# Optimization experiments

Hardware: AMD Instinct MI355X
Metric: run time of the kernel (lower is better)

## Reference

```python
import jax, jax.numpy as jnp
import numpy as np

E, H, F = 8, 1024, 4096  # experts, hidden_size, ffn_hidden_size
INIT_STD = 0.02


def setup_inputs() -> dict:
    key = jax.random.key(0)
    kx, k1, k2 = jax.random.split(key, 3)
    total_tokens = 16384
    x = jax.random.normal(kx, (total_tokens, H), dtype=jnp.float32)
    w1 = jax.random.normal(k1, (E, H, F), dtype=jnp.float32) * INIT_STD
    w2 = jax.random.normal(k2, (E, F, H), dtype=jnp.float32) * INIT_STD
    return {"x": x, "w1": w1, "w2": w2, "rows_per_expert": total_tokens // E}


def reference(x, w1, w2, rows_per_expert):
    # Grouped GEMM 1: per-expert x_e @ w1[e]  -> [E, T, F]
    e, h = w1.shape[0], w1.shape[1]
    xg = x.reshape(e, rows_per_expert, h)          # tokens grouped by expert
    inter = jnp.einsum('eth,ehf->etf', xg, w1)     # grouped GEMM 1
    inter = jax.nn.gelu(inter)                     # activation_fn
    out = jnp.einsum('etf,efh->eth', inter, w2)    # grouped GEMM 2
    return out.reshape(-1, h)
```

## Files before the change

### kernel.cpp

```cpp
#include <hip/hip_runtime.h>
#include <hip/hip_bf16.h>


typedef __attribute__((ext_vector_type(8))) short short8;
typedef __attribute__((ext_vector_type(4))) float floatx4;

static __device__ __forceinline__ ushort f2bf(float f) {
  __hip_bfloat16 h = __float2bfloat16(f);
  return *(ushort*)&h;
}

__global__ __launch_bounds__(256) void cvt_bf16(const float* __restrict__ in,
                                                __hip_bfloat16* __restrict__ out,
                                                int n4) {
  int i = blockIdx.x * 256 + threadIdx.x;
  if (i >= n4) return;
  float4 v = ((const float4*)in)[i];
  ushort4 u;
  u.x = f2bf(v.x); u.y = f2bf(v.y); u.z = f2bf(v.z); u.w = f2bf(v.w);
  ((ushort4*)out)[i] = u;
}

template<int K, int N>
__global__ __launch_bounds__(256) void tpose_bf16(const float* __restrict__ in,
                                                  __hip_bfloat16* __restrict__ out) {
  __shared__ __align__(16) ushort tile[64][66];
  const size_t eoff = (size_t)blockIdx.z * (size_t)K * N;
  const int n0 = blockIdx.x * 64;
  const int k0 = blockIdx.y * 64;
  const int t = threadIdx.x;
  const int g = t >> 4;
  const int j = t & 15;
#pragma unroll
  for (int p = 0; p < 2; ++p) {
    const int k = p * 32 + g * 2;
    const float4 a = *(const float4*)(in + eoff + (size_t)(k0 + k) * N + n0 + 4 * j);
    const float4 b = *(const float4*)(in + eoff + (size_t)(k0 + k + 1) * N + n0 + 4 * j);
#pragma unroll
    for (int i = 0; i < 4; ++i) {
      ushort2 u;
      u.x = f2bf(((const float*)&a)[i]);
      u.y = f2bf(((const float*)&b)[i]);
      *(ushort2*)&tile[4 * j + i][k] = u;
    }
  }
  __syncthreads();
#pragma unroll
  for (int p = 0; p < 4; ++p) {
    const int n = p * 16 + g;
    const ushort4 u = *(const ushort4*)&tile[n][4 * j];
    *(ushort4*)(out + eoff + (size_t)(n0 + n) * K + k0 + 4 * j) = u;
  }
}

template<bool GELU, typename OutT>
__global__ __launch_bounds__(256) void gemm_bt(const __hip_bfloat16* __restrict__ A,
                                               const __hip_bfloat16* __restrict__ Bt,
                                               OutT* __restrict__ C,
                                               int M, int N, int K) {
  __shared__ __align__(16) __hip_bfloat16 As[128 * 32];
  __shared__ __align__(16) __hip_bfloat16 Bs[128 * 32];

  const int e = blockIdx.z;
  A  += (size_t)e * M * K;
  Bt += (size_t)e * N * K;
  C  += (size_t)e * M * N;

  const int m0 = blockIdx.y * 128;
  const int n0 = blockIdx.x * 128;
  const int t = threadIdx.x;
  const int lane = t & 63;
  const int l16 = lane & 15;
  const int quad = lane >> 4;
  const int w = t >> 6;
  const int wr = (w >> 1) * 64;
  const int wc = (w & 1) * 64;

  floatx4 acc[4][4] = {};

  for (int k0 = 0; k0 < K; k0 += 32) {
    __syncthreads();
#pragma unroll
    for (int i = 0; i < 2; ++i) {
      const int id = t + i * 256;
      const int row = id >> 2;
      const int cc = (id & 3) * 8;
      __builtin_amdgcn_global_load_lds(
          (const __attribute__((address_space(1))) void*)(A + (size_t)(m0 + row) * K + k0 + cc),
          (__attribute__((address_space(3))) void*)(As + id * 8), 16, 0, 0);
    }
#pragma unroll
    for (int i = 0; i < 2; ++i) {
      const int id = t + i * 256;
      const int row = id >> 2;
      const int cc = (id & 3) * 8;
      __builtin_amdgcn_global_load_lds(
          (const __attribute__((address_space(1))) void*)(Bt + (size_t)(n0 + row) * K + k0 + cc),
          (__attribute__((address_space(3))) void*)(Bs + id * 8), 16, 0, 0);
    }
    __syncthreads();

    short8 af[4], bf[4];
#pragma unroll
    for (int i = 0; i < 4; ++i)
      af[i] = *(const short8*)(As + (wr + i * 16 + l16) * 32 + quad * 8);
#pragma unroll
    for (int j = 0; j < 4; ++j)
      bf[j] = *(const short8*)(Bs + (wc + j * 16 + l16) * 32 + quad * 8);
#pragma unroll
    for (int i = 0; i < 4; ++i)
#pragma unroll
      for (int j = 0; j < 4; ++j)
        acc[i][j] = __builtin_amdgcn_mfma_f32_16x16x32_bf16(af[i], bf[j], acc[i][j], 0, 0, 0);
  }

#pragma unroll
  for (int i = 0; i < 4; ++i) {
#pragma unroll
    for (int r = 0; r < 4; ++r) {
      const int row = m0 + wr + i * 16 + quad * 4 + r;
      OutT* crow = C + (size_t)row * N + n0 + wc + l16;
#pragma unroll
      for (int j = 0; j < 4; ++j) {
        float v = acc[i][j][r];
        if constexpr (GELU) {
          const float u2 = 1.5957691216057308f * (v + 0.044715f * v * v * v);
          const float ex = __expf(u2);
          v = v - v * __builtin_amdgcn_rcpf(ex + 1.0f);
        }
        if constexpr (sizeof(OutT) == 2)
          crow[j * 16] = __float2bfloat16(v);
        else
          crow[j * 16] = v;
      }
    }
  }
}

extern "C" void kernel_launch(void* const* d_in, const int* in_sizes, int n_in,
                              void* d_out, int out_size, void* d_ws, size_t ws_size,
                              hipStream_t stream) {
  const float* x  = (const float*)d_in[0];
  const float* w1 = (const float*)d_in[1];
  const float* w2 = (const float*)d_in[2];
  float* out = (float*)d_out;

  char* ws = (char*)d_ws;
  __hip_bfloat16* xb    = (__hip_bfloat16*)(ws);
  __hip_bfloat16* w1t   = (__hip_bfloat16*)(ws + (size_t)32 * 1024 * 1024);
  __hip_bfloat16* w2t   = (__hip_bfloat16*)(ws + (size_t)96 * 1024 * 1024);
  __hip_bfloat16* inter = (__hip_bfloat16*)(ws + (size_t)160 * 1024 * 1024);

  cvt_bf16<<<16384, 256, 0, stream>>>(x, xb, 16384 * 1024 / 4);
  tpose_bf16<1024, 4096><<<dim3(64, 16, 8), 256, 0, stream>>>(w1, w1t);
  tpose_bf16<4096, 1024><<<dim3(16, 64, 8), 256, 0, stream>>>(w2, w2t);
  gemm_bt<true, __hip_bfloat16>
      <<<dim3(32, 16, 8), 256, 0, stream>>>(xb, w1t, inter, 2048, 4096, 1024);
  gemm_bt<false, float>
      <<<dim3(8, 16, 8), 256, 0, stream>>>(inter, w2t, out, 2048, 1024, 4096);
}
```

Before: 760.8 us.

## Fuse input conversion and weight transposes into one prep kernel with swizzled LDS

Replaces the three separate preprocessing launches (x conversion, w1 transpose, w2 transpose) with one prep kernel that dispatches on block index. The transpose tiles grow to 128x64, each thread packs 8 bf16 values along K into a 16-byte store, and an XOR swizzle on the LDS layout replaces padding to avoid bank conflicts. This is meant to cut launch overhead and tail effects and to widen global stores, at the cost of more registers per thread and a larger shared-memory footprint per block.

```diff
diff --git a/kernel.cpp b/kernel.cpp
--- a/kernel.cpp
+++ b/kernel.cpp
@@ -10,46 +10,76 @@
   return *(ushort*)&h;
 }
 
-__global__ __launch_bounds__(256) void cvt_bf16(const float* __restrict__ in,
-                                                __hip_bfloat16* __restrict__ out,
-                                                int n4) {
-  int i = blockIdx.x * 256 + threadIdx.x;
-  if (i >= n4) return;
-  float4 v = ((const float4*)in)[i];
-  ushort4 u;
-  u.x = f2bf(v.x); u.y = f2bf(v.y); u.z = f2bf(v.z); u.w = f2bf(v.w);
-  ((ushort4*)out)[i] = u;
+static __device__ __forceinline__ int swz(int n, int o) {
+  return o ^ (n & 7) ^ ((n >> 3) & 7);
 }
 
 template<int K, int N>
-__global__ __launch_bounds__(256) void tpose_bf16(const float* __restrict__ in,
-                                                  __hip_bfloat16* __restrict__ out) {
-  __shared__ __align__(16) ushort tile[64][66];
-  const size_t eoff = (size_t)blockIdx.z * (size_t)K * N;
-  const int n0 = blockIdx.x * 64;
-  const int k0 = blockIdx.y * 64;
+static __device__ __forceinline__ void tpose_tile(const float* __restrict__ in,
+                                                  __hip_bfloat16* __restrict__ out,
+                                                  ushort* lds, int e, int nt, int kt) {
+  const size_t eoff = (size_t)e * K * N;
+  const int n0 = nt * 128, k0 = kt * 64;
   const int t = threadIdx.x;
+  const int j = t & 15;
   const int g = t >> 4;
-  const int j = t & 15;
+  const int o = g >> 1;
+  const int h = g & 1;
+  const float* src = in + eoff + (size_t)(k0 + 8 * o) * N + n0 + h * 64 + 4 * j;
+  float4 v[8];
 #pragma unroll
-  for (int p = 0; p < 2; ++p) {
-    const int k = p * 32 + g * 2;
-    const float4 a = *(const float4*)(in + eoff + (size_t)(k0 + k) * N + n0 + 4 * j);
-    const float4 b = *(const float4*)(in + eoff + (size_t)(k0 + k + 1) * N + n0 + 4 * j);
+  for (int r = 0; r < 8; ++r)
+    v[r] = *(const float4*)(src + (size_t)r * N);
 #pragma unroll
-    for (int i = 0; i < 4; ++i) {
-      ushort2 u;
-      u.x = f2bf(((const float*)&a)[i]);
-      u.y = f2bf(((const float*)&b)[i]);
-      *(ushort2*)&tile[4 * j + i][k] = u;
-    }
+  for (int i = 0; i < 4; ++i) {
+    const int n = h * 64 + 4 * j + i;
+    union { short8 s8; ushort u[8]; } p;
+#pragma unroll
+    for (int r = 0; r < 8; ++r)
+      p.u[r] = f2bf(((const float*)&v[r])[i]);
+    *(short8*)(lds + n * 64 + swz(n, o) * 8) = p.s8;
   }
   __syncthreads();
+  const int c = t & 7;
+  const int r0 = t >> 3;
 #pragma unroll
   for (int p = 0; p < 4; ++p) {
-    const int n = p * 16 + g;
-    const ushort4 u = *(const ushort4*)&tile[n][4 * j];
-    *(ushort4*)(out + eoff + (size_t)(n0 + n) * K + k0 + 4 * j) = u;
+    const int n = p * 32 + r0;
+    short8 u = *(const short8*)(lds + n * 64 + swz(n, c) * 8);
+    *(short8*)(out + eoff + (size_t)(n0 + n) * K + k0 + 8 * c) = u;
+  }
+}
+
+static __device__ __forceinline__ void cvt_part(const float* __restrict__ x,
+                                                __hip_bfloat16* __restrict__ xb, int b) {
+  const int t = threadIdx.x;
+  const float4* src = (const float4*)x + (size_t)b * 2048 + t;
+  ushort4* dst = (ushort4*)xb + (size_t)b * 2048 + t;
+#pragma unroll
+  for (int u = 0; u < 8; ++u) {
+    float4 v = src[u * 256];
+    ushort4 q;
+    q.x = f2bf(v.x); q.y = f2bf(v.y); q.z = f2bf(v.z); q.w = f2bf(v.w);
+    dst[u * 256] = q;
+  }
+}
+
+__global__ __launch_bounds__(256) void prep(const float* __restrict__ x,
+                                            const float* __restrict__ w1,
+                                            const float* __restrict__ w2,
+                                            __hip_bfloat16* __restrict__ xb,
+                                            __hip_bfloat16* __restrict__ w1t,
+                                            __hip_bfloat16* __restrict__ w2t) {
+  __shared__ __align__(16) ushort lds[128 * 64];
+  const int b = blockIdx.x;
+  if (b < 2048) {
+    cvt_part(x, xb, b);
+  } else if (b < 6144) {
+    const int bb = b - 2048;
+    tpose_tile<1024, 4096>(w1, w1t, lds, bb >> 9, bb & 31, (bb >> 5) & 15);
+  } else {
+    const int bb = b - 6144;
+    tpose_tile<4096, 1024>(w2, w2t, lds, bb >> 9, bb & 7, (bb >> 3) & 63);
   }
 }
 
@@ -151,9 +181,7 @@
   __hip_bfloat16* w2t   = (__hip_bfloat16*)(ws + (size_t)96 * 1024 * 1024);
   __hip_bfloat16* inter = (__hip_bfloat16*)(ws + (size_t)160 * 1024 * 1024);
 
-  cvt_bf16<<<16384, 256, 0, stream>>>(x, xb, 16384 * 1024 / 4);
-  tpose_bf16<1024, 4096><<<dim3(64, 16, 8), 256, 0, stream>>>(w1, w1t);
-  tpose_bf16<4096, 1024><<<dim3(16, 64, 8), 256, 0, stream>>>(w2, w2t);
+  prep<<<10240, 256, 0, stream>>>(x, w1, w2, xb, w1t, w2t);
   gemm_bt<true, __hip_bfloat16>
       <<<dim3(32, 16, 8), 256, 0, stream>>>(xb, w1t, inter, 2048, 4096, 1024);
   gemm_bt<false, float>
```

Measured after the change: 754.1 us. Within noise of the previous version (-0.9%).
